# Optimization experiments

Hardware: AMD Instinct MI355X
Metric: run time of the kernel (lower is better)

## Reference

```python
import jax, jax.numpy as jnp
import numpy as np

N = 131072
IN_F = 3
HID = 256
OUT_F = 3
GRID = 64
OMEGA = 30.0
LN_EPS = 1e-5


def setup_inputs() -> dict:
    key = jax.random.key(0)
    ks = jax.random.split(key, 16)
    coords = jax.random.uniform(ks[0], (N, IN_F), dtype=jnp.float32)
    # FourierKAN coeffs: randn / (sqrt(in) * sqrt(grid))
    fc = jax.random.normal(ks[1], (2, HID, IN_F, GRID), dtype=jnp.float32) / (np.sqrt(IN_F) * np.sqrt(GRID))
    ln_g = jnp.ones((HID,), jnp.float32)
    ln_b = jnp.zeros((HID,), jnp.float32)
    def sine_init(k, fan_in, fan_out):
        lim = np.sqrt(6.0 / fan_in) / OMEGA
        return jax.random.uniform(k, (fan_out, fan_in), jnp.float32, -lim, lim)
    w1 = sine_init(ks[2], HID, 2 * HID)
    b1 = jnp.zeros((2 * HID,), jnp.float32)
    w2 = sine_init(ks[3], 2 * HID, 2 * HID)
    b2 = jnp.zeros((2 * HID,), jnp.float32)
    w3 = sine_init(ks[4], 2 * HID, 2 * HID)
    b3 = jnp.zeros((2 * HID,), jnp.float32)
    w4 = sine_init(ks[5], 2 * HID, 4 * HID)
    b4 = jnp.zeros((4 * HID,), jnp.float32)
    lim_o = np.sqrt(6.0 / HID) / OMEGA
    wout = jax.random.uniform(ks[6], (OUT_F, 4 * HID), jnp.float32, -lim_o, lim_o)
    bout = jnp.zeros((OUT_F,), jnp.float32)
    fkan_bias = jnp.zeros((1, HID), jnp.float32)
    return dict(coords=coords, fc=fc, fkan_bias=fkan_bias, ln_g=ln_g, ln_b=ln_b,
                w1=w1, b1=b1, w2=w2, b2=b2, w3=w3, b3=b3, w4=w4, b4=b4,
                wout=wout, bout=bout)


def _fourier_kan(x, fc, bias):
    # x: (N, in). k: (grid,) = 1..grid. Features cos/sin(k*x): (N, in, grid).
    k = jnp.arange(1, GRID + 1, dtype=x.dtype)
    ang = x[:, :, None] * k  # (N, in, grid)
    # GEMM form of the broadcast-multiply-reduce in the original module
    y = jnp.einsum('nig,oig->no', jnp.cos(ang), fc[0])
    y = y + jnp.einsum('nig,oig->no', jnp.sin(ang), fc[1])
    return y + bias


def _layernorm(x, g, b):
    mu = jnp.mean(x, axis=-1, keepdims=True)
    var = jnp.mean((x - mu) ** 2, axis=-1, keepdims=True)
    return (x - mu) * jax.lax.rsqrt(var + LN_EPS) * g + b


def _sine_layer(x, w, b):
    z = x @ w.T + b
    return (z + jnp.tanh(OMEGA * z)) * jax.nn.sigmoid(z)


def reference(coords, fc, fkan_bias, ln_g, ln_b, w1, b1, w2, b2, w3, b3, w4, b4, wout, bout):
    x = _fourier_kan(coords, fc, fkan_bias)
    x = _layernorm(x, ln_g, ln_b)
    y = _sine_layer(x, w1, b1)
    y = _sine_layer(y, w2, b2)
    y = _sine_layer(y, w3, b3)
    y = _sine_layer(y, w4, b4)
    return y @ wout.T + bout
```

## Files before the change

kernel.cpp:

```cpp
#include <hip/hip_runtime.h>
#include <math.h>

#define N_PTS 131072
#define HID 256
#define H2 512
#define H4 1024
#define GRIDW 64
#define K1 384
#define TILE 128
#define LN_EPS 1e-5f
#define OMEGA 30.0f

typedef __bf16 b16x8 __attribute__((ext_vector_type(8)));
typedef __bf16 b16x4 __attribute__((ext_vector_type(4)));
typedef float f32x4 __attribute__((ext_vector_type(4)));

#define OFF_FC 0
#define N_FC   (HID * K1)
#define OFF_W1 (OFF_FC + N_FC)
#define N_W1   (H2 * HID)
#define OFF_W2 (OFF_W1 + N_W1)
#define N_W2   (H2 * H2)
#define OFF_W3 (OFF_W2 + N_W2)
#define OFF_W4 (OFF_W3 + N_W2)
#define N_W4   (H4 * H2)
#define N_TOTAL (OFF_W4 + N_W4)

__global__ void prep_kernel(const float* __restrict__ fc, const float* __restrict__ w1,
                            const float* __restrict__ w2, const float* __restrict__ w3,
                            const float* __restrict__ w4, __bf16* __restrict__ ws) {
  int idx = blockIdx.x * blockDim.x + threadIdx.x;
  if (idx >= N_TOTAL) return;
  int r, K, NK;
  const float* src = nullptr;
  int region;
  if (idx < OFF_W1)      { r = idx - OFF_FC; K = K1;  region = 0; }
  else if (idx < OFF_W2) { r = idx - OFF_W1; K = HID; src = w1; region = 1; }
  else if (idx < OFF_W3) { r = idx - OFF_W2; K = H2;  src = w2; region = 1; }
  else if (idx < OFF_W4) { r = idx - OFF_W3; K = H2;  src = w3; region = 1; }
  else                   { r = idx - OFF_W4; K = H2;  src = w4; region = 1; }
  NK = K / 32;
  int c = r >> 9, p = r & 511;
  int otile = c / NK, ks = c % NK;
  int lane = p >> 3, j = p & 7;
  int o = otile * 16 + (lane & 15);
  int k = ks * 32 + ((lane >> 4) << 3) + j;
  float v;
  if (region == 0) {
    int s = k / 192, rem = k % 192, i = rem / GRIDW, g = rem % GRIDW;
    v = fc[((s * HID + o) * 3 + i) * GRIDW + g];
  } else {
    v = src[o * K + k];
  }
  ws[idx] = (__bf16)v;
}


__device__ __forceinline__ float actfn(float z) {
  const float L2E = 1.4426950408889634f;
  float t2 = __builtin_amdgcn_exp2f((2.0f * OMEGA * L2E) * z);
  float th = 1.0f - 2.0f * __builtin_amdgcn_rcpf(t2 + 1.0f);
  float se = __builtin_amdgcn_exp2f(-L2E * z);
  float sg = __builtin_amdgcn_rcpf(1.0f + se);
  return (z + th) * sg;
}

__device__ __forceinline__ void fast_sincos(float ang, float* s, float* c) {
  const float INV2PI = 0.15915493667125702f;
  float r = __builtin_amdgcn_fractf(ang * INV2PI);
  *s = __builtin_amdgcn_sinf(r);
  *c = __builtin_amdgcn_cosf(r);
}

#define SWZ(n) (((n) & 15) << 4)

template <int K, int OT>
__device__ __forceinline__ void gemm_kloop(const unsigned char* sX, const __bf16* __restrict__ W,
                                           int lane, int o_base, f32x4 (&acc)[OT][8]) {
  const int l15 = lane & 15, lh = lane >> 4;
  constexpr int NK = K / 32;
  b16x8 wf[OT];
#pragma unroll
  for (int ot = 0; ot < OT; ++ot)
    wf[ot] = *(const b16x8*)(W + (size_t)((o_base / 16 + ot) * NK) * 512 + lane * 8);
#pragma unroll 1
  for (int ks = 0; ks < NK; ++ks) {
    b16x8 xf[8];
#pragma unroll
    for (int nt = 0; nt < 8; ++nt) {
      int n = nt * 16 + l15;
      int kb = ks * 64 + (lh << 4);
      xf[nt] = *(const b16x8*)(sX + n * 1024 + (kb ^ SWZ(n)));
    }
    b16x8 wn[OT];
    if (ks + 1 < NK) {
#pragma unroll
      for (int ot = 0; ot < OT; ++ot)
        wn[ot] = *(const b16x8*)(W + (size_t)((o_base / 16 + ot) * NK + ks + 1) * 512 + lane * 8);
    }
#pragma unroll
    for (int ot = 0; ot < OT; ++ot)
#pragma unroll
      for (int nt = 0; nt < 8; ++nt)
        acc[ot][nt] = __builtin_amdgcn_mfma_f32_16x16x32_bf16(wf[ot], xf[nt], acc[ot][nt], 0, 0, 0);
#pragma unroll
    for (int ot = 0; ot < OT; ++ot) wf[ot] = wn[ot];
  }
}

template <int K>
__device__ __forceinline__ void sine_layer_ip(unsigned char* sAct,
                                              const __bf16* __restrict__ W,
                                              const float* __restrict__ bias, int lane, int wid) {
  f32x4 acc[4][8] = {};
  const int o_base = wid * 64;
  gemm_kloop<K, 4>(sAct, W, lane, o_base, acc);
  const int l15 = lane & 15, lh = lane >> 4;
  __syncthreads();
#pragma unroll
  for (int ot = 0; ot < 4; ++ot) {
    int o0 = o_base + ot * 16 + (lh << 2);
    f32x4 bia = *(const f32x4*)(bias + o0);
#pragma unroll
    for (int nt = 0; nt < 8; ++nt) {
      int n = nt * 16 + l15;
      b16x4 h;
      h[0] = (__bf16)actfn(acc[ot][nt][0] + bia[0]);
      h[1] = (__bf16)actfn(acc[ot][nt][1] + bia[1]);
      h[2] = (__bf16)actfn(acc[ot][nt][2] + bia[2]);
      h[3] = (__bf16)actfn(acc[ot][nt][3] + bia[3]);
      *(b16x4*)(sAct + n * 1024 + ((o0 * 2) ^ SWZ(n))) = h;
    }
  }
  __syncthreads();
}

__global__ __launch_bounds__(512, 2) void fkan_inr_kernel(
    const float* __restrict__ coords, const float* __restrict__ fkan_bias,
    const float* __restrict__ ln_g, const float* __restrict__ ln_b,
    const float* __restrict__ b1, const float* __restrict__ b2,
    const float* __restrict__ b3, const float* __restrict__ b4,
    const float* __restrict__ wout, const float* __restrict__ bout,
    const __bf16* __restrict__ ws, float* __restrict__ out) {
  __shared__ __align__(16) unsigned char sAct[TILE * 1024];
  __shared__ float sSum[TILE], sSqs[TILE];
  __shared__ float sOutF[TILE][4];

  const int tid = threadIdx.x;
  const int lane = tid & 63, wid = tid >> 6;
  const int l15 = lane & 15, lh = lane >> 4;
  const int base_n = blockIdx.x * TILE;

  if (tid < TILE) {
    sSum[tid] = 0.f; sSqs[tid] = 0.f;
    sOutF[tid][0] = 0.f; sOutF[tid][1] = 0.f; sOutF[tid][2] = 0.f; sOutF[tid][3] = 0.f;
  }
#pragma unroll
  for (int p = 0; p < 6; ++p) {
    int id = tid + p * 512;
    int n = id / 24, rem = id % 24, i = rem >> 3, g0 = (rem & 7) * 8;
    float c = coords[(base_n + n) * 3 + i];
    b16x8 cv, sv;
#pragma unroll
    for (int j = 0; j < 8; ++j) {
      float ang = c * (float)(g0 + j + 1);
      float s, co;
      fast_sincos(ang, &s, &co);
      cv[j] = (__bf16)co;
      sv[j] = (__bf16)s;
    }
    int kc = (i * GRIDW + g0) * 2;
    *(b16x8*)(sAct + n * 1024 + (kc ^ SWZ(n))) = cv;
    int ks2 = (192 + i * GRIDW + g0) * 2;
    *(b16x8*)(sAct + n * 1024 + (ks2 ^ SWZ(n))) = sv;
  }
  __syncthreads();

  {
    f32x4 acc[2][8] = {};
    const int o_base = wid * 32;
    gemm_kloop<K1, 2>(sAct, ws + OFF_FC, lane, o_base, acc);
#pragma unroll
    for (int ot = 0; ot < 2; ++ot) {
      int o0 = o_base + ot * 16 + (lh << 2);
      f32x4 bia = *(const f32x4*)(fkan_bias + o0);
#pragma unroll
      for (int nt = 0; nt < 8; ++nt) acc[ot][nt] += bia;
    }
#pragma unroll
    for (int nt = 0; nt < 8; ++nt) {
      float s = 0.f, q = 0.f;
#pragma unroll
      for (int ot = 0; ot < 2; ++ot)
#pragma unroll
        for (int r = 0; r < 4; ++r) { float z = acc[ot][nt][r]; s += z; q += z * z; }
      s += __shfl_xor(s, 16); q += __shfl_xor(q, 16);
      s += __shfl_xor(s, 32); q += __shfl_xor(q, 32);
      if (lane < 16) {
        atomicAdd(&sSum[nt * 16 + lane], s);
        atomicAdd(&sSqs[nt * 16 + lane], q);
      }
    }
    __syncthreads();
#pragma unroll
    for (int nt = 0; nt < 8; ++nt) {
      int n = nt * 16 + l15;
      float mu = sSum[n] * (1.f / HID);
      float var = sSqs[n] * (1.f / HID) - mu * mu;
      float rs = rsqrtf(var + LN_EPS);
#pragma unroll
      for (int ot = 0; ot < 2; ++ot) {
        int o0 = o_base + ot * 16 + (lh << 2);
        f32x4 g4 = *(const f32x4*)(ln_g + o0);
        f32x4 bb = *(const f32x4*)(ln_b + o0);
        b16x4 h;
        h[0] = (__bf16)((acc[ot][nt][0] - mu) * rs * g4[0] + bb[0]);
        h[1] = (__bf16)((acc[ot][nt][1] - mu) * rs * g4[1] + bb[1]);
        h[2] = (__bf16)((acc[ot][nt][2] - mu) * rs * g4[2] + bb[2]);
        h[3] = (__bf16)((acc[ot][nt][3] - mu) * rs * g4[3] + bb[3]);
        *(b16x4*)(sAct + n * 1024 + ((o0 * 2) ^ SWZ(n))) = h;
      }
    }
    __syncthreads();
  }

  sine_layer_ip<HID>(sAct, ws + OFF_W1, b1, lane, wid);
  sine_layer_ip<H2>(sAct, ws + OFF_W2, b2, lane, wid);
  sine_layer_ip<H2>(sAct, ws + OFF_W3, b3, lane, wid);

  {
#pragma unroll 1
    for (int pass = 0; pass < 2; ++pass) {
      f32x4 acc[4][8] = {};
      int o_base = pass * 512 + wid * 64;
      gemm_kloop<H2, 4>(sAct, ws + OFF_W4, lane, o_base, acc);
      float pj[8][3] = {};
#pragma unroll
      for (int ot = 0; ot < 4; ++ot) {
        int o0 = o_base + ot * 16 + (lh << 2);
        f32x4 bia = *(const f32x4*)(b4 + o0);
        f32x4 wo0 = *(const f32x4*)(wout + 0 * H4 + o0);
        f32x4 wo1 = *(const f32x4*)(wout + 1 * H4 + o0);
        f32x4 wo2 = *(const f32x4*)(wout + 2 * H4 + o0);
#pragma unroll
        for (int nt = 0; nt < 8; ++nt) {
          float a0 = actfn(acc[ot][nt][0] + bia[0]);
          float a1 = actfn(acc[ot][nt][1] + bia[1]);
          float a2 = actfn(acc[ot][nt][2] + bia[2]);
          float a3 = actfn(acc[ot][nt][3] + bia[3]);
          pj[nt][0] += a0 * wo0[0] + a1 * wo0[1] + a2 * wo0[2] + a3 * wo0[3];
          pj[nt][1] += a0 * wo1[0] + a1 * wo1[1] + a2 * wo1[2] + a3 * wo1[3];
          pj[nt][2] += a0 * wo2[0] + a1 * wo2[1] + a2 * wo2[2] + a3 * wo2[3];
        }
      }
#pragma unroll
      for (int nt = 0; nt < 8; ++nt)
#pragma unroll
        for (int j = 0; j < 3; ++j) {
          float r = pj[nt][j];
          r += __shfl_xor(r, 16);
          r += __shfl_xor(r, 32);
          if (lane < 16) atomicAdd(&sOutF[nt * 16 + lane][j], r);
        }
    }
    __syncthreads();
    if (tid < TILE * 3) {
      int n = tid / 3, j = tid % 3;
      out[(base_n + n) * 3 + j] = sOutF[n][j] + bout[j];
    }
  }
}

extern "C" void kernel_launch(void* const* d_in, const int* in_sizes, int n_in,
                              void* d_out, int out_size, void* d_ws, size_t ws_size,
                              hipStream_t stream) {
  const float* coords    = (const float*)d_in[0];
  const float* fc        = (const float*)d_in[1];
  const float* fkan_bias = (const float*)d_in[2];
  const float* ln_g      = (const float*)d_in[3];
  const float* ln_b      = (const float*)d_in[4];
  const float* w1        = (const float*)d_in[5];
  const float* b1        = (const float*)d_in[6];
  const float* w2        = (const float*)d_in[7];
  const float* b2        = (const float*)d_in[8];
  const float* w3        = (const float*)d_in[9];
  const float* b3        = (const float*)d_in[10];
  const float* w4        = (const float*)d_in[11];
  const float* b4        = (const float*)d_in[12];
  const float* wout      = (const float*)d_in[13];
  const float* bout      = (const float*)d_in[14];
  float* out = (float*)d_out;
  __bf16* ws = (__bf16*)d_ws;

  prep_kernel<<<(N_TOTAL + 255) / 256, 256, 0, stream>>>(fc, w1, w2, w3, w4, ws);
  fkan_inr_kernel<<<N_PTS / TILE, 512, 0, stream>>>(coords, fkan_bias, ln_g, ln_b,
                                                    b1, b2, b3, b4, wout, bout, ws, out);
}
```

Measured before the change: 392.7 us.

## Split tile into two row halves and overlap epilogues with next GEMM

The 128-row tile is split into two 64-row halves with separate accumulator sets. The activation epilogue (LayerNorm, sine activation, output projection) of one half is interleaved in quarter chunks between the k-loop segments of the other half's GEMM. The aim is to hide the transcendental VALU work behind MFMA work instead of running them back to back. Weight prefetching is dropped and each weight fragment is now reloaded once per half, doubling global and L2 weight traffic. More code and live accumulators may also raise register pressure.

New measurement: 896.4 us. 128% more time.

```diff
diff --git a/kernel.cpp b/kernel.cpp
--- a/kernel.cpp
+++ b/kernel.cpp
@@ -31,7 +31,7 @@
                             const float* __restrict__ w4, __bf16* __restrict__ ws) {
   int idx = blockIdx.x * blockDim.x + threadIdx.x;
   if (idx >= N_TOTAL) return;
-  int r, K, NK;
+  int r, K;
   const float* src = nullptr;
   int region;
   if (idx < OFF_W1)      { r = idx - OFF_FC; K = K1;  region = 0; }
@@ -39,7 +39,7 @@
   else if (idx < OFF_W3) { r = idx - OFF_W2; K = H2;  src = w2; region = 1; }
   else if (idx < OFF_W4) { r = idx - OFF_W3; K = H2;  src = w3; region = 1; }
   else                   { r = idx - OFF_W4; K = H2;  src = w4; region = 1; }
-  NK = K / 32;
+  int NK = K / 32;
   int c = r >> 9, p = r & 511;
   int otile = c / NK, ks = c % NK;
   int lane = p >> 3, j = p & 7;
@@ -55,7 +55,6 @@
   ws[idx] = (__bf16)v;
 }
 
-
 __device__ __forceinline__ float actfn(float z) {
   const float L2E = 1.4426950408889634f;
   float t2 = __builtin_amdgcn_exp2f((2.0f * OMEGA * L2E) * z);
@@ -74,65 +73,116 @@
 
 #define SWZ(n) (((n) & 15) << 4)
 
-template <int K, int OT>
-__device__ __forceinline__ void gemm_kloop(const unsigned char* sX, const __bf16* __restrict__ W,
-                                           int lane, int o_base, f32x4 (&acc)[OT][8]) {
+template <int K, int OT, int KS0, int KS1>
+__device__ __forceinline__ void gemm_range(const unsigned char* sX, int hbase,
+                                           const __bf16* __restrict__ W,
+                                           int lane, int o_base, f32x4 (&acc)[4][4]) {
   const int l15 = lane & 15, lh = lane >> 4;
   constexpr int NK = K / 32;
-  b16x8 wf[OT];
-#pragma unroll
-  for (int ot = 0; ot < OT; ++ot)
-    wf[ot] = *(const b16x8*)(W + (size_t)((o_base / 16 + ot) * NK) * 512 + lane * 8);
 #pragma unroll 1
-  for (int ks = 0; ks < NK; ++ks) {
-    b16x8 xf[8];
-#pragma unroll
-    for (int nt = 0; nt < 8; ++nt) {
-      int n = nt * 16 + l15;
+  for (int ks = KS0; ks < KS1; ++ks) {
+    b16x8 xf[4];
+#pragma unroll
+    for (int nt = 0; nt < 4; ++nt) {
+      int n = hbase + nt * 16 + l15;
       int kb = ks * 64 + (lh << 4);
       xf[nt] = *(const b16x8*)(sX + n * 1024 + (kb ^ SWZ(n)));
     }
-    b16x8 wn[OT];
-    if (ks + 1 < NK) {
-#pragma unroll
-      for (int ot = 0; ot < OT; ++ot)
-        wn[ot] = *(const b16x8*)(W + (size_t)((o_base / 16 + ot) * NK + ks + 1) * 512 + lane * 8);
-    }
+    b16x8 wf[OT];
 #pragma unroll
     for (int ot = 0; ot < OT; ++ot)
-#pragma unroll
-      for (int nt = 0; nt < 8; ++nt)
+      wf[ot] = *(const b16x8*)(W + (size_t)((o_base / 16 + ot) * NK + ks) * 512 + lane * 8);
+#pragma unroll
+    for (int ot = 0; ot < OT; ++ot)
+#pragma unroll
+      for (int nt = 0; nt < 4; ++nt)
         acc[ot][nt] = __builtin_amdgcn_mfma_f32_16x16x32_bf16(wf[ot], xf[nt], acc[ot][nt], 0, 0, 0);
-#pragma unroll
-    for (int ot = 0; ot < OT; ++ot) wf[ot] = wn[ot];
-  }
-}
-
-template <int K>
-__device__ __forceinline__ void sine_layer_ip(unsigned char* sAct,
-                                              const __bf16* __restrict__ W,
-                                              const float* __restrict__ bias, int lane, int wid) {
-  f32x4 acc[4][8] = {};
-  const int o_base = wid * 64;
-  gemm_kloop<K, 4>(sAct, W, lane, o_base, acc);
+  }
+}
+
+template <int U0, int U1>
+__device__ __forceinline__ void sineE_units(unsigned char* sAct, f32x4 (&acc)[4][4],
+                                            const float* __restrict__ bias,
+                                            int hbase, int o_base, int lane) {
   const int l15 = lane & 15, lh = lane >> 4;
-  __syncthreads();
-#pragma unroll
-  for (int ot = 0; ot < 4; ++ot) {
+#pragma unroll
+  for (int u = U0; u < U1; ++u) {
+    int ot = u >> 2, nt = u & 3;
     int o0 = o_base + ot * 16 + (lh << 2);
     f32x4 bia = *(const f32x4*)(bias + o0);
-#pragma unroll
-    for (int nt = 0; nt < 8; ++nt) {
-      int n = nt * 16 + l15;
-      b16x4 h;
-      h[0] = (__bf16)actfn(acc[ot][nt][0] + bia[0]);
-      h[1] = (__bf16)actfn(acc[ot][nt][1] + bia[1]);
-      h[2] = (__bf16)actfn(acc[ot][nt][2] + bia[2]);
-      h[3] = (__bf16)actfn(acc[ot][nt][3] + bia[3]);
-      *(b16x4*)(sAct + n * 1024 + ((o0 * 2) ^ SWZ(n))) = h;
-    }
-  }
-  __syncthreads();
+    int n = hbase + nt * 16 + l15;
+    b16x4 h;
+    h[0] = (__bf16)actfn(acc[ot][nt][0] + bia[0]);
+    h[1] = (__bf16)actfn(acc[ot][nt][1] + bia[1]);
+    h[2] = (__bf16)actfn(acc[ot][nt][2] + bia[2]);
+    h[3] = (__bf16)actfn(acc[ot][nt][3] + bia[3]);
+    *(b16x4*)(sAct + n * 1024 + ((o0 * 2) ^ SWZ(n))) = h;
+  }
+}
+
+template <int U0, int U1>
+__device__ __forceinline__ void lnE_units(unsigned char* sAct, f32x4 (&acc)[4][4],
+                                          const float* sSum, const float* sSqs,
+                                          const float* __restrict__ ln_g,
+                                          const float* __restrict__ ln_b,
+                                          int hbase, int o_base, int lane) {
+  const int l15 = lane & 15, lh = lane >> 4;
+#pragma unroll
+  for (int u = U0; u < U1; ++u) {
+    int ot = u >> 2, nt = u & 3;
+    int n = hbase + nt * 16 + l15;
+    float mu = sSum[n] * (1.f / HID);
+    float var = sSqs[n] * (1.f / HID) - mu * mu;
+    float rs = rsqrtf(var + LN_EPS);
+    int o0 = o_base + ot * 16 + (lh << 2);
+    f32x4 g4 = *(const f32x4*)(ln_g + o0);
+    f32x4 bb = *(const f32x4*)(ln_b + o0);
+    b16x4 h;
+    h[0] = (__bf16)((acc[ot][nt][0] - mu) * rs * g4[0] + bb[0]);
+    h[1] = (__bf16)((acc[ot][nt][1] - mu) * rs * g4[1] + bb[1]);
+    h[2] = (__bf16)((acc[ot][nt][2] - mu) * rs * g4[2] + bb[2]);
+    h[3] = (__bf16)((acc[ot][nt][3] - mu) * rs * g4[3] + bb[3]);
+    *(b16x4*)(sAct + n * 1024 + ((o0 * 2) ^ SWZ(n))) = h;
+  }
+}
+
+template <int U0, int U1>
+__device__ __forceinline__ void l4E_units(f32x4 (&acc)[4][4], const float* __restrict__ b4,
+                                          const float* __restrict__ wout, int o_base,
+                                          float (&pj)[4][3], int lane) {
+  const int lh = lane >> 4;
+#pragma unroll
+  for (int u = U0; u < U1; ++u) {
+    int ot = u >> 2, nt = u & 3;
+    int o0 = o_base + ot * 16 + (lh << 2);
+    f32x4 bia = *(const f32x4*)(b4 + o0);
+    f32x4 wo0 = *(const f32x4*)(wout + 0 * H4 + o0);
+    f32x4 wo1 = *(const f32x4*)(wout + 1 * H4 + o0);
+    f32x4 wo2 = *(const f32x4*)(wout + 2 * H4 + o0);
+    float a0 = actfn(acc[ot][nt][0] + bia[0]);
+    float a1 = actfn(acc[ot][nt][1] + bia[1]);
+    float a2 = actfn(acc[ot][nt][2] + bia[2]);
+    float a3 = actfn(acc[ot][nt][3] + bia[3]);
+    pj[nt][0] += a0 * wo0[0] + a1 * wo0[1] + a2 * wo0[2] + a3 * wo0[3];
+    pj[nt][1] += a0 * wo1[0] + a1 * wo1[1] + a2 * wo1[2] + a3 * wo1[3];
+    pj[nt][2] += a0 * wo2[0] + a1 * wo2[1] + a2 * wo2[2] + a3 * wo2[3];
+  }
+}
+
+template <int K, int OT, class E0, class E1, class E2, class E3>
+__device__ __forceinline__ void phaseG(unsigned char* sAct, const __bf16* __restrict__ W,
+                                       int hbase, int o_base, int lane, f32x4 (&acc)[4][4],
+                                       E0&& e0, E1&& e1, E2&& e2, E3&& e3) {
+  constexpr int NK = K / 32;
+  f32x4 zv = {0.f, 0.f, 0.f, 0.f};
+#pragma unroll
+  for (int ot = 0; ot < OT; ++ot)
+#pragma unroll
+    for (int nt = 0; nt < 4; ++nt) acc[ot][nt] = zv;
+  gemm_range<K, OT, 0, NK / 4>(sAct, hbase, W, lane, o_base, acc);           e0();
+  gemm_range<K, OT, NK / 4, NK / 2>(sAct, hbase, W, lane, o_base, acc);      e1();
+  gemm_range<K, OT, NK / 2, 3 * NK / 4>(sAct, hbase, W, lane, o_base, acc);  e2();
+  gemm_range<K, OT, 3 * NK / 4, NK>(sAct, hbase, W, lane, o_base, acc);      e3();
 }
 
 __global__ __launch_bounds__(512, 2) void fkan_inr_kernel(
@@ -176,98 +226,138 @@
   }
   __syncthreads();
 
-  {
-    f32x4 acc[2][8] = {};
-    const int o_base = wid * 32;
-    gemm_kloop<K1, 2>(sAct, ws + OFF_FC, lane, o_base, acc);
-#pragma unroll
-    for (int ot = 0; ot < 2; ++ot) {
-      int o0 = o_base + ot * 16 + (lh << 2);
-      f32x4 bia = *(const f32x4*)(fkan_bias + o0);
-#pragma unroll
-      for (int nt = 0; nt < 8; ++nt) acc[ot][nt] += bia;
+  f32x4 accA[4][4], accB[4][4];
+  auto NOP = [&] {};
+
+  phaseG<K1, 2>(sAct, ws + OFF_FC, 0, wid * 32, lane, accA, NOP, NOP, NOP, NOP);
+#pragma unroll
+  for (int ot = 0; ot < 2; ++ot) {
+    int o0 = wid * 32 + ot * 16 + (lh << 2);
+    f32x4 bia = *(const f32x4*)(fkan_bias + o0);
+#pragma unroll
+    for (int nt = 0; nt < 4; ++nt) accA[ot][nt] += bia;
+  }
+#pragma unroll
+  for (int nt = 0; nt < 4; ++nt) {
+    float s = 0.f, q = 0.f;
+#pragma unroll
+    for (int ot = 0; ot < 2; ++ot)
+#pragma unroll
+      for (int r = 0; r < 4; ++r) { float z = accA[ot][nt][r]; s += z; q += z * z; }
+    s += __shfl_xor(s, 16); q += __shfl_xor(q, 16);
+    s += __shfl_xor(s, 32); q += __shfl_xor(q, 32);
+    if (lane < 16) { atomicAdd(&sSum[nt * 16 + lane], s); atomicAdd(&sSqs[nt * 16 + lane], q); }
+  }
+  __syncthreads();
+
+  phaseG<K1, 2>(sAct, ws + OFF_FC, 64, wid * 32, lane, accB,
+    [&] { lnE_units<0, 2>(sAct, accA, sSum, sSqs, ln_g, ln_b, 0, wid * 32, lane); },
+    [&] { lnE_units<2, 4>(sAct, accA, sSum, sSqs, ln_g, ln_b, 0, wid * 32, lane); },
+    [&] { lnE_units<4, 6>(sAct, accA, sSum, sSqs, ln_g, ln_b, 0, wid * 32, lane); },
+    [&] { lnE_units<6, 8>(sAct, accA, sSum, sSqs, ln_g, ln_b, 0, wid * 32, lane); });
+#pragma unroll
+  for (int ot = 0; ot < 2; ++ot) {
+    int o0 = wid * 32 + ot * 16 + (lh << 2);
+    f32x4 bia = *(const f32x4*)(fkan_bias + o0);
+#pragma unroll
+    for (int nt = 0; nt < 4; ++nt) accB[ot][nt] += bia;
+  }
+#pragma unroll
+  for (int nt = 0; nt < 4; ++nt) {
+    float s = 0.f, q = 0.f;
+#pragma unroll
+    for (int ot = 0; ot < 2; ++ot)
+#pragma unroll
+      for (int r = 0; r < 4; ++r) { float z = accB[ot][nt][r]; s += z; q += z * z; }
+    s += __shfl_xor(s, 16); q += __shfl_xor(q, 16);
+    s += __shfl_xor(s, 32); q += __shfl_xor(q, 32);
+    if (lane < 16) { atomicAdd(&sSum[64 + nt * 16 + lane], s); atomicAdd(&sSqs[64 + nt * 16 + lane], q); }
+  }
+  __syncthreads();
+
+  phaseG<HID, 4>(sAct, ws + OFF_W1, 0, wid * 64, lane, accA,
+    [&] { lnE_units<0, 2>(sAct, accB, sSum, sSqs, ln_g, ln_b, 64, wid * 32, lane); },
+    [&] { lnE_units<2, 4>(sAct, accB, sSum, sSqs, ln_g, ln_b, 64, wid * 32, lane); },
+    [&] { lnE_units<4, 6>(sAct, accB, sSum, sSqs, ln_g, ln_b, 64, wid * 32, lane); },
+    [&] { lnE_units<6, 8>(sAct, accB, sSum, sSqs, ln_g, ln_b, 64, wid * 32, lane); });
+  __syncthreads();
+
+  phaseG<HID, 4>(sAct, ws + OFF_W1, 64, wid * 64, lane, accB,
+    [&] { sineE_units<0, 4>(sAct, accA, b1, 0, wid * 64, lane); },
+    [&] { sineE_units<4, 8>(sAct, accA, b1, 0, wid * 64, lane); },
+    [&] { sineE_units<8, 12>(sAct, accA, b1, 0, wid * 64, lane); },
+    [&] { sineE_units<12, 16>(sAct, accA, b1, 0, wid * 64, lane); });
+  __syncthreads();
+
+  phaseG<H2, 4>(sAct, ws + OFF_W2, 0, wid * 64, lane, accA,
+    [&] { sineE_units<0, 4>(sAct, accB, b1, 64, wid * 64, lane); },
+    [&] { sineE_units<4, 8>(sAct, accB, b1, 64, wid * 64, lane); },
+    [&] { sineE_units<8, 12>(sAct, accB, b1, 64, wid * 64, lane); },
+    [&] { sineE_units<12, 16>(sAct, accB, b1, 64, wid * 64, lane); });
+  __syncthreads();
+
+  phaseG<H2, 4>(sAct, ws + OFF_W2, 64, wid * 64, lane, accB,
+    [&] { sineE_units<0, 4>(sAct, accA, b2, 0, wid * 64, lane); },
+    [&] { sineE_units<4, 8>(sAct, accA, b2, 0, wid * 64, lane); },
+    [&] { sineE_units<8, 12>(sAct, accA, b2, 0, wid * 64, lane); },
+    [&] { sineE_units<12, 16>(sAct, accA, b2, 0, wid * 64, lane); });
+  __syncthreads();
+
+  phaseG<H2, 4>(sAct, ws + OFF_W3, 0, wid * 64, lane, accA,
+    [&] { sineE_units<0, 4>(sAct, accB, b2, 64, wid * 64, lane); },
+    [&] { sineE_units<4, 8>(sAct, accB, b2, 64, wid * 64, lane); },
+    [&] { sineE_units<8, 12>(sAct, accB, b2, 64, wid * 64, lane); },
+    [&] { sineE_units<12, 16>(sAct, accB, b2, 64, wid * 64, lane); });
+  __syncthreads();
+
+  phaseG<H2, 4>(sAct, ws + OFF_W3, 64, wid * 64, lane, accB,
+    [&] { sineE_units<0, 4>(sAct, accA, b3, 0, wid * 64, lane); },
+    [&] { sineE_units<4, 8>(sAct, accA, b3, 0, wid * 64, lane); },
+    [&] { sineE_units<8, 12>(sAct, accA, b3, 0, wid * 64, lane); },
+    [&] { sineE_units<12, 16>(sAct, accA, b3, 0, wid * 64, lane); });
+  __syncthreads();
+
+  phaseG<H2, 4>(sAct, ws + OFF_W4, 0, wid * 64, lane, accA,
+    [&] { sineE_units<0, 4>(sAct, accB, b3, 64, wid * 64, lane); },
+    [&] { sineE_units<4, 8>(sAct, accB, b3, 64, wid * 64, lane); },
+    [&] { sineE_units<8, 12>(sAct, accB, b3, 64, wid * 64, lane); },
+    [&] { sineE_units<12, 16>(sAct, accB, b3, 64, wid * 64, lane); });
+  __syncthreads();
+
+  float pjA[4][3] = {};
+  float pjB[4][3] = {};
+  phaseG<H2, 4>(sAct, ws + OFF_W4, 64, wid * 64, lane, accB,
+    [&] { l4E_units<0, 4>(accA, b4, wout, wid * 64, pjA, lane); },
+    [&] { l4E_units<4, 8>(accA, b4, wout, wid * 64, pjA, lane); },
+    [&] { l4E_units<8, 12>(accA, b4, wout, wid * 64, pjA, lane); },
+    [&] { l4E_units<12, 16>(accA, b4, wout, wid * 64, pjA, lane); });
+  phaseG<H2, 4>(sAct, ws + OFF_W4, 0, 512 + wid * 64, lane, accA,
+    [&] { l4E_units<0, 4>(accB, b4, wout, wid * 64, pjB, lane); },
+    [&] { l4E_units<4, 8>(accB, b4, wout, wid * 64, pjB, lane); },
+    [&] { l4E_units<8, 12>(accB, b4, wout, wid * 64, pjB, lane); },
+    [&] { l4E_units<12, 16>(accB, b4, wout, wid * 64, pjB, lane); });
+  phaseG<H2, 4>(sAct, ws + OFF_W4, 64, 512 + wid * 64, lane, accB,
+    [&] { l4E_units<0, 4>(accA, b4, wout, 512 + wid * 64, pjA, lane); },
+    [&] { l4E_units<4, 8>(accA, b4, wout, 512 + wid * 64, pjA, lane); },
+    [&] { l4E_units<8, 12>(accA, b4, wout, 512 + wid * 64, pjA, lane); },
+    [&] { l4E_units<12, 16>(accA, b4, wout, 512 + wid * 64, pjA, lane); });
+  l4E_units<0, 16>(accB, b4, wout, 512 + wid * 64, pjB, lane);
+
+#pragma unroll
+  for (int nt = 0; nt < 4; ++nt)
+#pragma unroll
+    for (int j = 0; j < 3; ++j) {
+      float r = pjA[nt][j];
+      r += __shfl_xor(r, 16); r += __shfl_xor(r, 32);
+      if (lane < 16) atomicAdd(&sOutF[nt * 16 + lane][j], r);
+      float rb = pjB[nt][j];
+      rb += __shfl_xor(rb, 16); rb += __shfl_xor(rb, 32);
+      if (lane < 16) atomicAdd(&sOutF[64 + nt * 16 + lane][j], rb);
     }
-#pragma unroll
-    for (int nt = 0; nt < 8; ++nt) {
-      float s = 0.f, q = 0.f;
-#pragma unroll
-      for (int ot = 0; ot < 2; ++ot)
-#pragma unroll
-        for (int r = 0; r < 4; ++r) { float z = acc[ot][nt][r]; s += z; q += z * z; }
-      s += __shfl_xor(s, 16); q += __shfl_xor(q, 16);
-      s += __shfl_xor(s, 32); q += __shfl_xor(q, 32);
-      if (lane < 16) {
-        atomicAdd(&sSum[nt * 16 + lane], s);
-        atomicAdd(&sSqs[nt * 16 + lane], q);
-      }
-    }
-    __syncthreads();
-#pragma unroll
-    for (int nt = 0; nt < 8; ++nt) {
-      int n = nt * 16 + l15;
-      float mu = sSum[n] * (1.f / HID);
-      float var = sSqs[n] * (1.f / HID) - mu * mu;
-      float rs = rsqrtf(var + LN_EPS);
-#pragma unroll
-      for (int ot = 0; ot < 2; ++ot) {
-        int o0 = o_base + ot * 16 + (lh << 2);
-        f32x4 g4 = *(const f32x4*)(ln_g + o0);
-        f32x4 bb = *(const f32x4*)(ln_b + o0);
-        b16x4 h;
-        h[0] = (__bf16)((acc[ot][nt][0] - mu) * rs * g4[0] + bb[0]);
-        h[1] = (__bf16)((acc[ot][nt][1] - mu) * rs * g4[1] + bb[1]);
-        h[2] = (__bf16)((acc[ot][nt][2] - mu) * rs * g4[2] + bb[2]);
-        h[3] = (__bf16)((acc[ot][nt][3] - mu) * rs * g4[3] + bb[3]);
-        *(b16x4*)(sAct + n * 1024 + ((o0 * 2) ^ SWZ(n))) = h;
-      }
-    }
-    __syncthreads();
-  }
-
-  sine_layer_ip<HID>(sAct, ws + OFF_W1, b1, lane, wid);
-  sine_layer_ip<H2>(sAct, ws + OFF_W2, b2, lane, wid);
-  sine_layer_ip<H2>(sAct, ws + OFF_W3, b3, lane, wid);
-
-  {
-#pragma unroll 1
-    for (int pass = 0; pass < 2; ++pass) {
-      f32x4 acc[4][8] = {};
-      int o_base = pass * 512 + wid * 64;
-      gemm_kloop<H2, 4>(sAct, ws + OFF_W4, lane, o_base, acc);
-      float pj[8][3] = {};
-#pragma unroll
-      for (int ot = 0; ot < 4; ++ot) {
-        int o0 = o_base + ot * 16 + (lh << 2);
-        f32x4 bia = *(const f32x4*)(b4 + o0);
-        f32x4 wo0 = *(const f32x4*)(wout + 0 * H4 + o0);
-        f32x4 wo1 = *(const f32x4*)(wout + 1 * H4 + o0);
-        f32x4 wo2 = *(const f32x4*)(wout + 2 * H4 + o0);
-#pragma unroll
-        for (int nt = 0; nt < 8; ++nt) {
-          float a0 = actfn(acc[ot][nt][0] + bia[0]);
-          float a1 = actfn(acc[ot][nt][1] + bia[1]);
-          float a2 = actfn(acc[ot][nt][2] + bia[2]);
-          float a3 = actfn(acc[ot][nt][3] + bia[3]);
-          pj[nt][0] += a0 * wo0[0] + a1 * wo0[1] + a2 * wo0[2] + a3 * wo0[3];
-          pj[nt][1] += a0 * wo1[0] + a1 * wo1[1] + a2 * wo1[2] + a3 * wo1[3];
-          pj[nt][2] += a0 * wo2[0] + a1 * wo2[1] + a2 * wo2[2] + a3 * wo2[3];
-        }
-      }
-#pragma unroll
-      for (int nt = 0; nt < 8; ++nt)
-#pragma unroll
-        for (int j = 0; j < 3; ++j) {
-          float r = pj[nt][j];
-          r += __shfl_xor(r, 16);
-          r += __shfl_xor(r, 32);
-          if (lane < 16) atomicAdd(&sOutF[nt * 16 + lane][j], r);
-        }
-    }
-    __syncthreads();
-    if (tid < TILE * 3) {
-      int n = tid / 3, j = tid % 3;
-      out[(base_n + n) * 3 + j] = sOutF[n][j] + bout[j];
-    }
+  __syncthreads();
+  if (tid < TILE * 3) {
+    int n = tid / 3, j = tid % 3;
+    out[(base_n + n) * 3 + j] = sOutF[n][j] + bout[j];
   }
 }
 
```
